# Kernel optimization log

Measured on AMD Instinct MI355X. Metric: run time of the kernel, lower is better.

The kernel has to match this reference:

```python
import jax, jax.numpy as jnp
import numpy as np

VOCAB = 1_000_000
D = 128
N = 16384
NSAMP = 8192
TEMP = 0.05
L2_NORM = True


def _l2n(x):
    return x / (jnp.linalg.norm(x, axis=-1, keepdims=True) + 1e-12)


def setup_inputs() -> dict:
    key = jax.random.key(0)
    k1, k2, k3, k4, k5 = jax.random.split(key, 5)
    inputs = jax.random.normal(k1, (N, D), dtype=jnp.float32)
    target_ids = jax.random.randint(k2, (N, 1), 0, VOCAB, dtype=jnp.int64) if jax.config.jax_enable_x64 else jax.random.randint(k2, (N, 1), 0, VOCAB, dtype=jnp.int32)
    neg_ids = jax.random.randint(k3, (NSAMP,), 0, VOCAB, dtype=jnp.int32)
    weights = jax.random.uniform(k4, (N,), dtype=jnp.float32)
    projection = jax.random.normal(k5, (VOCAB, D), dtype=jnp.float32) * 0.02
    return {"inputs": inputs, "target_ids": target_ids, "neg_ids": neg_ids,
            "weights": weights, "projection": projection}


def reference(inputs, target_ids, neg_ids, weights, projection):
    # mask = (target_ids != -100).sum(-1).bool(); instead of dynamic boolean
    # indexing, fold the mask into the per-example weights (same weighted mean).
    valid = ((target_ids != -100).sum(axis=-1) > 0).astype(inputs.dtype)  # [N]
    tgt = jnp.clip(target_ids[:, 0], 0, VOCAB - 1)  # safe gather for masked rows

    pos_emb = projection[tgt]       # [N, D] gather
    neg_emb = projection[neg_ids]   # [S, D] gather

    x = inputs
    if L2_NORM:
        x = _l2n(x)
        pos_emb = _l2n(pos_emb)
        neg_emb = _l2n(neg_emb)

    pos_logit = jnp.einsum('nd,nd->n', x, pos_emb) / TEMP          # [N]
    neg_logits = jnp.einsum('nd,sd->ns', x, neg_emb) / TEMP        # [N, S]

    logits = jnp.concatenate([pos_logit[:, None], neg_logits], axis=-1)  # [N, 1+S]
    logZ = jax.scipy.special.logsumexp(logits, axis=-1)            # [N]
    ce = logZ - pos_logit                                          # -log p(pos)

    w = weights * valid
    loss = jnp.sum(ce * w) / jnp.maximum(jnp.sum(w), 1e-12)
    return loss
```

## Files before the change

### kernel.cpp

```cpp
#include <hip/hip_runtime.h>
#include <hip/hip_bf16.h>
#include <stdint.h>
#include <math.h>

#define VOCAB 1000000
#define D 128
#define NROWS 16384
#define NSAMP 8192
#define SSPLIT 8
#define K1F 28.853900817779268f
#define LOG2EF 1.4426950408889634f

#define XF_OFF 0u
#define EF_OFF 4194304u
#define PL_OFF 6291456u
#define PS_OFF 6356992u
#define FP_OFF 6881280u
#define CNT_OFF 6882304u

typedef __attribute__((ext_vector_type(8))) __bf16 bf16x8;
typedef __attribute__((ext_vector_type(16))) float f32x16;

#if __has_builtin(__builtin_amdgcn_exp2f)
#define EXP2(x) __builtin_amdgcn_exp2f(x)
#else
#define EXP2(x) exp2f(x)
#endif

__device__ __forceinline__ void gl_lds16(const void* g, void* l) {
  __builtin_amdgcn_global_load_lds(
      (const __attribute__((address_space(1))) unsigned int*)g,
      (__attribute__((address_space(3))) unsigned int*)l, 16, 0, 0);
}

__device__ __forceinline__ float wave_sum(float v) {
#pragma unroll
  for (int o = 1; o < 64; o <<= 1) v += __shfl_xor(v, o);
  return v;
}

__device__ __forceinline__ float expsum16(const f32x16& c) {
  float e[16];
#pragma unroll
  for (int r = 0; r < 16; ++r) e[r] = EXP2(c[r]);
#pragma unroll
  for (int s = 8; s; s >>= 1)
#pragma unroll
    for (int r = 0; r < s; ++r) e[r] += e[r + s];
  return e[0];
}

__device__ __forceinline__ void store_frag(__bf16* __restrict__ base, int row,
                                           int lane, float vx, float vy) {
  const int d = lane * 2;
  const int kk = d >> 4, sub = (d & 15) >> 3, j = d & 7;
  const int tile = row >> 5, lt = (sub << 5) | (row & 31);
  __bf16* dst = base + ((((size_t)tile * 8 + kk) * 64 + lt) * 8 + j);
  dst[0] = (__bf16)vx;
  dst[1] = (__bf16)vy;
}

__global__ __launch_bounds__(256) void prep_kernel(
    const float* __restrict__ x, const int* __restrict__ tgt,
    const int* __restrict__ nid, const float* __restrict__ proj,
    __bf16* __restrict__ xf, __bf16* __restrict__ ef,
    float* __restrict__ pl, unsigned int* __restrict__ cnt) {
  if (blockIdx.x == 0 && threadIdx.x == 0) *cnt = 0u;
  const int wave = threadIdx.x >> 6, lane = threadIdx.x & 63;
  if (blockIdx.x < 1024) {
    const int n0 = blockIdx.x * 16 + wave * 4;
    int tg[4];
    float2 xr[4], pr[4];
#pragma unroll
    for (int i = 0; i < 4; ++i) {
      const int t = tgt[n0 + i];
      tg[i] = t < 0 ? 0 : (t > VOCAB - 1 ? VOCAB - 1 : t);
      xr[i] = *reinterpret_cast<const float2*>(x + (size_t)(n0 + i) * D + lane * 2);
    }
#pragma unroll
    for (int i = 0; i < 4; ++i)
      pr[i] = *reinterpret_cast<const float2*>(proj + (size_t)tg[i] * D + lane * 2);
#pragma unroll
    for (int i = 0; i < 4; ++i) {
      float sx = xr[i].x * xr[i].x + xr[i].y * xr[i].y;
      float sp = pr[i].x * pr[i].x + pr[i].y * pr[i].y;
      float dt = xr[i].x * pr[i].x + xr[i].y * pr[i].y;
#pragma unroll
      for (int o = 1; o < 64; o <<= 1) {
        sx += __shfl_xor(sx, o);
        sp += __shfl_xor(sp, o);
        dt += __shfl_xor(dt, o);
      }
      const float rnx = 1.f / (sqrtf(sx) + 1e-12f);
      if (lane == 0)
        pl[n0 + i] = dt * rnx * (1.f / (sqrtf(sp) + 1e-12f)) * 20.0f;
      const float sc = rnx * K1F;
      store_frag(xf, n0 + i, lane, xr[i].x * sc, xr[i].y * sc);
    }
  } else {
    const int s0 = (blockIdx.x - 1024) * 16 + wave * 4;
    float2 er[4];
#pragma unroll
    for (int i = 0; i < 4; ++i) {
      const int id = nid[s0 + i];
      er[i] = *reinterpret_cast<const float2*>(proj + (size_t)id * D + lane * 2);
    }
#pragma unroll
    for (int i = 0; i < 4; ++i) {
      const float rn =
          1.f / (sqrtf(wave_sum(er[i].x * er[i].x + er[i].y * er[i].y)) + 1e-12f);
      store_frag(ef, s0 + i, lane, er[i].x * rn, er[i].y * rn);
    }
  }
}

__global__ __launch_bounds__(256, 3) void flash_kernel(
    const __bf16* __restrict__ xf, const __bf16* __restrict__ ef,
    float* __restrict__ psum) {
  __shared__ __align__(16) char lds[2][16384];
  const int tid = threadIdx.x, wave = tid >> 6, lane = tid & 63;
  const int nb = blockIdx.x & 63, ss = blockIdx.x >> 6;

  bf16x8 bq[2][8];
#pragma unroll
  for (int nf = 0; nf < 2; ++nf) {
    const __bf16* p = xf + ((size_t)(nb * 8 + wave * 2 + nf) * 4096) + lane * 8;
#pragma unroll
    for (int kk = 0; kk < 8; ++kk)
      bq[nf][kk] = *reinterpret_cast<const bf16x8*>(p + kk * 512);
  }

  const char* esrc = reinterpret_cast<const char*>(ef) + (size_t)ss * 262144;
  float acc0 = 0.f, acc1 = 0.f;

  {
    const char* g = esrc + wave * 1024 + lane * 16;
    char* l = &lds[0][0] + wave * 1024;
#pragma unroll
    for (int i = 0; i < 4; ++i) gl_lds16(g + i * 4096, l + i * 4096);
  }
  __syncthreads();

  for (int st = 0; st < 16; ++st) {
    if (st < 15) {
      const char* g = esrc + (size_t)(st + 1) * 16384 + wave * 1024 + lane * 16;
      char* l = &lds[(st + 1) & 1][0] + wave * 1024;
#pragma unroll
      for (int i = 0; i < 4; ++i) gl_lds16(g + i * 4096, l + i * 4096);
    }
    const char* cb = &lds[st & 1][0];
#pragma unroll
    for (int tt = 0; tt < 2; ++tt) {
      f32x16 c0, c1;
#pragma unroll
      for (int r = 0; r < 16; ++r) { c0[r] = 0.f; c1[r] = 0.f; }
      const char* ab = cb + tt * 8192 + lane * 16;
#pragma unroll
      for (int kk = 0; kk < 8; ++kk) {
        bf16x8 a = *reinterpret_cast<const bf16x8*>(ab + kk * 1024);
        c0 = __builtin_amdgcn_mfma_f32_32x32x16_bf16(a, bq[0][kk], c0, 0, 0, 0);
        c1 = __builtin_amdgcn_mfma_f32_32x32x16_bf16(a, bq[1][kk], c1, 0, 0, 0);
      }
      acc0 += expsum16(c0);
      acc1 += expsum16(c1);
    }
    __syncthreads();
  }

  acc0 += __shfl_xor(acc0, 32);
  acc1 += __shfl_xor(acc1, 32);
  if (lane < 32) {
    const int nbase = nb * 256 + wave * 64;
    psum[(size_t)ss * NROWS + nbase + lane] = acc0;
    psum[(size_t)ss * NROWS + nbase + 32 + lane] = acc1;
  }
}

__global__ __launch_bounds__(256) void finish_kernel(
    const float* __restrict__ psum, const float* __restrict__ pl,
    const int* __restrict__ tgt, const float* __restrict__ wts,
    float* __restrict__ fin, unsigned int* __restrict__ cnt,
    float* __restrict__ out) {
  const int n = blockIdx.x * 256 + threadIdx.x;
  float tot = 0.f;
#pragma unroll
  for (int s = 0; s < SSPLIT; ++s) tot += psum[(size_t)s * NROWS + n];
  const float p = pl[n];
  tot += EXP2(p * LOG2EF);
  const float ce = logf(tot) - p;
  const float w = wts[n] * (tgt[n] != -100 ? 1.f : 0.f);
  float a = wave_sum(ce * w);
  float b = wave_sum(w);
  __shared__ float sa[4], sb[4];
  __shared__ int last;
  const int wave = threadIdx.x >> 6, lane = threadIdx.x & 63;
  if (lane == 0) { sa[wave] = a; sb[wave] = b; }
  __syncthreads();
  if (threadIdx.x == 0) {
    __hip_atomic_store(&fin[blockIdx.x * 2], sa[0] + sa[1] + sa[2] + sa[3],
                       __ATOMIC_RELAXED, __HIP_MEMORY_SCOPE_AGENT);
    __hip_atomic_store(&fin[blockIdx.x * 2 + 1], sb[0] + sb[1] + sb[2] + sb[3],
                       __ATOMIC_RELAXED, __HIP_MEMORY_SCOPE_AGENT);
    const unsigned int old = __hip_atomic_fetch_add(cnt, 1u, __ATOMIC_ACQ_REL,
                                                    __HIP_MEMORY_SCOPE_AGENT);
    last = (old == 63u);
  }
  __syncthreads();
  if (last && threadIdx.x < 64) {
    const float A = wave_sum(__hip_atomic_load(&fin[threadIdx.x * 2],
                                               __ATOMIC_RELAXED,
                                               __HIP_MEMORY_SCOPE_AGENT));
    const float B = wave_sum(__hip_atomic_load(&fin[threadIdx.x * 2 + 1],
                                               __ATOMIC_RELAXED,
                                               __HIP_MEMORY_SCOPE_AGENT));
    if (threadIdx.x == 0) out[0] = A / fmaxf(B, 1e-12f);
  }
}

extern "C" void kernel_launch(void* const* d_in, const int* in_sizes, int n_in,
                              void* d_out, int out_size, void* d_ws, size_t ws_size,
                              hipStream_t stream) {
  const float* x    = (const float*)d_in[0];
  const int*   tgt  = (const int*)d_in[1];
  const int*   nid  = (const int*)d_in[2];
  const float* wts  = (const float*)d_in[3];
  const float* proj = (const float*)d_in[4];
  float* out = (float*)d_out;
  char* ws = (char*)d_ws;
  __bf16* xf = (__bf16*)(ws + XF_OFF);
  __bf16* ef = (__bf16*)(ws + EF_OFF);
  float* pl   = (float*)(ws + PL_OFF);
  float* psum = (float*)(ws + PS_OFF);
  float* fin  = (float*)(ws + FP_OFF);
  unsigned int* cnt = (unsigned int*)(ws + CNT_OFF);

  hipLaunchKernelGGL(prep_kernel, dim3(1024 + 512), dim3(256), 0, stream,
                     x, tgt, nid, proj, xf, ef, pl, cnt);
  hipLaunchKernelGGL(flash_kernel, dim3(64 * SSPLIT), dim3(256), 0, stream,
                     xf, ef, psum);
  hipLaunchKernelGGL(finish_kernel, dim3(NROWS / 256), dim3(256), 0, stream,
                     psum, pl, tgt, wts, fin, cnt, out);
}
```

Baseline: 49.36 us.

## Quantize normalized inputs and negatives to int8 and use i8 MFMA

Replaces the bf16 operands with int8 quantization. Each row of x gets its own absmax scale, and each negative embedding gets a fixed 127/norm scale. The logit matmul now uses mfma_i32_32x32x32_i8, with a per-row float rescale applied before exp2. This halves operand bytes and LDS traffic, doubles the K per MFMA, and raises the occupancy hint to 4 blocks. The risk is lower accuracy in the logits, which are scaled by 1/TEMP=20 before exponentiation, so quantization error could push the loss past tolerance.

```diff
diff --git a/kernel.cpp b/kernel.cpp
--- a/kernel.cpp
+++ b/kernel.cpp
@@ -12,14 +12,15 @@
 #define LOG2EF 1.4426950408889634f
 
 #define XF_OFF 0u
-#define EF_OFF 4194304u
-#define PL_OFF 6291456u
-#define PS_OFF 6356992u
-#define FP_OFF 6881280u
-#define CNT_OFF 6882304u
-
-typedef __attribute__((ext_vector_type(8))) __bf16 bf16x8;
-typedef __attribute__((ext_vector_type(16))) float f32x16;
+#define EF_OFF 2097152u
+#define PL_OFF 3145728u
+#define SCX_OFF 3211264u
+#define PS_OFF 3276800u
+#define FP_OFF 3801088u
+#define CNT_OFF 3802112u
+
+typedef __attribute__((ext_vector_type(4))) int i32x4;
+typedef __attribute__((ext_vector_type(16))) int i32x16;
 
 #if __has_builtin(__builtin_amdgcn_exp2f)
 #define EXP2(x) __builtin_amdgcn_exp2f(x)
@@ -39,32 +40,22 @@
   return v;
 }
 
-__device__ __forceinline__ float expsum16(const f32x16& c) {
-  float e[16];
-#pragma unroll
-  for (int r = 0; r < 16; ++r) e[r] = EXP2(c[r]);
-#pragma unroll
-  for (int s = 8; s; s >>= 1)
-#pragma unroll
-    for (int r = 0; r < s; ++r) e[r] += e[r + s];
-  return e[0];
-}
-
-__device__ __forceinline__ void store_frag(__bf16* __restrict__ base, int row,
-                                           int lane, float vx, float vy) {
+__device__ __forceinline__ void store_frag_i8(char* __restrict__ base, int row,
+                                              int lane, int bx, int by) {
   const int d = lane * 2;
-  const int kk = d >> 4, sub = (d & 15) >> 3, j = d & 7;
+  const int kk = d >> 5, sub = (d & 31) >> 4, j = d & 15;
   const int tile = row >> 5, lt = (sub << 5) | (row & 31);
-  __bf16* dst = base + ((((size_t)tile * 8 + kk) * 64 + lt) * 8 + j);
-  dst[0] = (__bf16)vx;
-  dst[1] = (__bf16)vy;
+  char* dst = base + (((size_t)(tile * 4 + kk) * 64 + lt) * 16 + j);
+  dst[0] = (char)bx;
+  dst[1] = (char)by;
 }
 
 __global__ __launch_bounds__(256) void prep_kernel(
     const float* __restrict__ x, const int* __restrict__ tgt,
     const int* __restrict__ nid, const float* __restrict__ proj,
-    __bf16* __restrict__ xf, __bf16* __restrict__ ef,
-    float* __restrict__ pl, unsigned int* __restrict__ cnt) {
+    char* __restrict__ xf, char* __restrict__ ef,
+    float* __restrict__ pl, float* __restrict__ scx,
+    unsigned int* __restrict__ cnt) {
   if (blockIdx.x == 0 && threadIdx.x == 0) *cnt = 0u;
   const int wave = threadIdx.x >> 6, lane = threadIdx.x & 63;
   if (blockIdx.x < 1024) {
@@ -85,17 +76,22 @@
       float sx = xr[i].x * xr[i].x + xr[i].y * xr[i].y;
       float sp = pr[i].x * pr[i].x + pr[i].y * pr[i].y;
       float dt = xr[i].x * pr[i].x + xr[i].y * pr[i].y;
+      float mx = fmaxf(fabsf(xr[i].x), fabsf(xr[i].y));
 #pragma unroll
       for (int o = 1; o < 64; o <<= 1) {
         sx += __shfl_xor(sx, o);
         sp += __shfl_xor(sp, o);
         dt += __shfl_xor(dt, o);
-      }
-      const float rnx = 1.f / (sqrtf(sx) + 1e-12f);
-      if (lane == 0)
-        pl[n0 + i] = dt * rnx * (1.f / (sqrtf(sp) + 1e-12f)) * 20.0f;
-      const float sc = rnx * K1F;
-      store_frag(xf, n0 + i, lane, xr[i].x * sc, xr[i].y * sc);
+        mx = fmaxf(mx, __shfl_xor(mx, o));
+      }
+      const float norm = sqrtf(sx) + 1e-12f;
+      if (lane == 0) {
+        pl[n0 + i] = dt / (norm * (sqrtf(sp) + 1e-12f)) * 20.0f;
+        scx[n0 + i] = K1F * (mx + 1e-20f) / (16129.0f * norm);
+      }
+      const float qs = 127.0f / (mx + 1e-20f);
+      store_frag_i8(xf, n0 + i, lane, (int)rintf(xr[i].x * qs),
+                    (int)rintf(xr[i].y * qs));
     }
   } else {
     const int s0 = (blockIdx.x - 1024) * 16 + wave * 4;
@@ -107,62 +103,76 @@
     }
 #pragma unroll
     for (int i = 0; i < 4; ++i) {
-      const float rn =
-          1.f / (sqrtf(wave_sum(er[i].x * er[i].x + er[i].y * er[i].y)) + 1e-12f);
-      store_frag(ef, s0 + i, lane, er[i].x * rn, er[i].y * rn);
-    }
-  }
-}
-
-__global__ __launch_bounds__(256, 3) void flash_kernel(
-    const __bf16* __restrict__ xf, const __bf16* __restrict__ ef,
-    float* __restrict__ psum) {
-  __shared__ __align__(16) char lds[2][16384];
+      const float qs =
+          127.0f / (sqrtf(wave_sum(er[i].x * er[i].x + er[i].y * er[i].y)) + 1e-12f);
+      store_frag_i8(ef, s0 + i, lane, (int)rintf(er[i].x * qs),
+                    (int)rintf(er[i].y * qs));
+    }
+  }
+}
+
+__global__ __launch_bounds__(256, 4) void flash_kernel(
+    const char* __restrict__ xf, const char* __restrict__ ef,
+    const float* __restrict__ scx, float* __restrict__ psum) {
+  __shared__ __align__(16) char lds[2][8192];
   const int tid = threadIdx.x, wave = tid >> 6, lane = tid & 63;
   const int nb = blockIdx.x & 63, ss = blockIdx.x >> 6;
-
-  bf16x8 bq[2][8];
+  const int nbase = nb * 256 + wave * 64;
+
+  i32x4 bq[2][4];
 #pragma unroll
   for (int nf = 0; nf < 2; ++nf) {
-    const __bf16* p = xf + ((size_t)(nb * 8 + wave * 2 + nf) * 4096) + lane * 8;
-#pragma unroll
-    for (int kk = 0; kk < 8; ++kk)
-      bq[nf][kk] = *reinterpret_cast<const bf16x8*>(p + kk * 512);
-  }
-
-  const char* esrc = reinterpret_cast<const char*>(ef) + (size_t)ss * 262144;
+    const char* p = xf + ((size_t)(nb * 8 + wave * 2 + nf) * 4096) + lane * 16;
+#pragma unroll
+    for (int kk = 0; kk < 4; ++kk)
+      bq[nf][kk] = *reinterpret_cast<const i32x4*>(p + kk * 1024);
+  }
+  const float scx0 = scx[nbase + (lane & 31)];
+  const float scx1 = scx[nbase + 32 + (lane & 31)];
+
+  const char* esrc = ef + (size_t)ss * 131072;
   float acc0 = 0.f, acc1 = 0.f;
 
   {
-    const char* g = esrc + wave * 1024 + lane * 16;
-    char* l = &lds[0][0] + wave * 1024;
-#pragma unroll
-    for (int i = 0; i < 4; ++i) gl_lds16(g + i * 4096, l + i * 4096);
+    const char* g = esrc + tid * 16;
+    char* l = &lds[0][0] + tid * 16;
+    gl_lds16(g, l);
+    gl_lds16(g + 4096, l + 4096);
   }
   __syncthreads();
 
   for (int st = 0; st < 16; ++st) {
     if (st < 15) {
-      const char* g = esrc + (size_t)(st + 1) * 16384 + wave * 1024 + lane * 16;
-      char* l = &lds[(st + 1) & 1][0] + wave * 1024;
-#pragma unroll
-      for (int i = 0; i < 4; ++i) gl_lds16(g + i * 4096, l + i * 4096);
+      const char* g = esrc + (size_t)(st + 1) * 8192 + tid * 16;
+      char* l = &lds[(st + 1) & 1][0] + tid * 16;
+      gl_lds16(g, l);
+      gl_lds16(g + 4096, l + 4096);
     }
     const char* cb = &lds[st & 1][0];
 #pragma unroll
     for (int tt = 0; tt < 2; ++tt) {
-      f32x16 c0, c1;
-#pragma unroll
-      for (int r = 0; r < 16; ++r) { c0[r] = 0.f; c1[r] = 0.f; }
-      const char* ab = cb + tt * 8192 + lane * 16;
-#pragma unroll
-      for (int kk = 0; kk < 8; ++kk) {
-        bf16x8 a = *reinterpret_cast<const bf16x8*>(ab + kk * 1024);
-        c0 = __builtin_amdgcn_mfma_f32_32x32x16_bf16(a, bq[0][kk], c0, 0, 0, 0);
-        c1 = __builtin_amdgcn_mfma_f32_32x32x16_bf16(a, bq[1][kk], c1, 0, 0, 0);
-      }
-      acc0 += expsum16(c0);
-      acc1 += expsum16(c1);
+      i32x16 c0, c1;
+#pragma unroll
+      for (int r = 0; r < 16; ++r) { c0[r] = 0; c1[r] = 0; }
+      const char* ab = cb + tt * 4096 + lane * 16;
+#pragma unroll
+      for (int kk = 0; kk < 4; ++kk) {
+        i32x4 a = *reinterpret_cast<const i32x4*>(ab + kk * 1024);
+        c0 = __builtin_amdgcn_mfma_i32_32x32x32_i8(a, bq[0][kk], c0, 0, 0, 0);
+        c1 = __builtin_amdgcn_mfma_i32_32x32x32_i8(a, bq[1][kk], c1, 0, 0, 0);
+      }
+      float e0[16], e1[16];
+#pragma unroll
+      for (int r = 0; r < 16; ++r) {
+        e0[r] = EXP2((float)c0[r] * scx0);
+        e1[r] = EXP2((float)c1[r] * scx1);
+      }
+#pragma unroll
+      for (int s2 = 8; s2; s2 >>= 1)
+#pragma unroll
+        for (int r = 0; r < s2; ++r) { e0[r] += e0[r + s2]; e1[r] += e1[r + s2]; }
+      acc0 += e0[0];
+      acc1 += e1[0];
     }
     __syncthreads();
   }
@@ -170,7 +180,6 @@
   acc0 += __shfl_xor(acc0, 32);
   acc1 += __shfl_xor(acc1, 32);
   if (lane < 32) {
-    const int nbase = nb * 256 + wave * 64;
     psum[(size_t)ss * NROWS + nbase + lane] = acc0;
     psum[(size_t)ss * NROWS + nbase + 32 + lane] = acc1;
   }
@@ -227,17 +236,18 @@
   const float* proj = (const float*)d_in[4];
   float* out = (float*)d_out;
   char* ws = (char*)d_ws;
-  __bf16* xf = (__bf16*)(ws + XF_OFF);
-  __bf16* ef = (__bf16*)(ws + EF_OFF);
+  char* xf = ws + XF_OFF;
+  char* ef = ws + EF_OFF;
   float* pl   = (float*)(ws + PL_OFF);
+  float* scx  = (float*)(ws + SCX_OFF);
   float* psum = (float*)(ws + PS_OFF);
   float* fin  = (float*)(ws + FP_OFF);
   unsigned int* cnt = (unsigned int*)(ws + CNT_OFF);
 
   hipLaunchKernelGGL(prep_kernel, dim3(1024 + 512), dim3(256), 0, stream,
-                     x, tgt, nid, proj, xf, ef, pl, cnt);
+                     x, tgt, nid, proj, xf, ef, pl, scx, cnt);
   hipLaunchKernelGGL(flash_kernel, dim3(64 * SSPLIT), dim3(256), 0, stream,
-                     xf, ef, psum);
+                     xf, ef, scx, psum);
   hipLaunchKernelGGL(finish_kernel, dim3(NROWS / 256), dim3(256), 0, stream,
                      psum, pl, tgt, wts, fin, cnt, out);
 }
```

Measured after the change: 42.72 us. 13.4% less time.
